# Kernel optimization log

Hardware: AMD Instinct MI355X
Metric: run time of the kernel (lower is better)

The kernel has to match this reference:

```python
import jax, jax.numpy as jnp
import numpy as np

EPS = 1e-05
NEG = -1000000000.0

def rmsnorm(x):
    var = jnp.mean(x * x, axis=-1, keepdims=True)
    return x * jax.lax.rsqrt(var + EPS)

def apply_rotary(x, cos, sin):
    # x: [B,T,H,D], cos/sin: [T,D]
    d = x.shape[-1]
    x1, x2 = x[..., : d // 2], x[..., d // 2 :]
    half_rot = jnp.concatenate([-x2, x1], axis=-1)
    c = cos[None, :, None, :]
    s = sin[None, :, None, :]
    return x * c + half_rot * s

def setup_inputs() -> dict:
    key = jax.random.key(0)
    ks = jax.random.split(key, 12)
    B, T, C, H = 2, 2048, 1024, 16
    hd = C // H
    std = 0.02
    return {
        "x": jax.random.normal(ks[0], (B, T, C), jnp.float32),
        "x0": jax.random.normal(ks[1], (B, T, C), jnp.float32),
        "lambdaResid": jnp.ones((), jnp.float32),
        "lambdaX0": jnp.ones((), jnp.float32),
        "cos": jax.random.uniform(ks[2], (T, hd), jnp.float32),
        "sin": jax.random.uniform(ks[3], (T, hd), jnp.float32),
        "qWeight": jax.random.normal(ks[4], (C, C), jnp.float32) * std,
        "kWeight": jax.random.normal(ks[5], (C, C), jnp.float32) * std,
        "vWeight": jax.random.normal(ks[6], (C, C), jnp.float32) * std,
        "projWeight": jax.random.normal(ks[7], (C, C), jnp.float32) * std,
        "fcWeight": jax.random.normal(ks[8], (C, 4 * C), jnp.float32) * std,
        "mlpProjWeight": jax.random.normal(ks[9], (4 * C, C), jnp.float32) * std,
    }

def reference(x, x0, lambdaResid, lambdaX0, cos, sin,
              qWeight, kWeight, vWeight, projWeight, fcWeight, mlpProjWeight):
    B, T, C = x.shape
    hd = cos.shape[-1]
    H = C // hd
    scaled = x * lambdaResid + x0 * lambdaX0
    pre = rmsnorm(scaled)
    q = (pre @ qWeight).reshape(B, T, H, hd)
    k = (pre @ kWeight).reshape(B, T, H, hd)
    v = (pre @ vWeight).reshape(B, T, H, hd)
    q = rmsnorm(apply_rotary(q, cos, sin))  # [B,T,H,D]
    k = rmsnorm(apply_rotary(k, cos, sin))
    scores = jnp.einsum('bthd,bshd->bhts', q, k) / jnp.sqrt(jnp.float32(hd))
    mask = jnp.tril(jnp.ones((T, T), bool))
    scores = jnp.where(mask[None, None], scores, NEG)
    probs = jax.nn.softmax(scores, axis=-1)
    attn = jnp.einsum('bhts,bshd->bthd', probs, v).reshape(B, T, C)
    scaled = scaled + attn @ projWeight
    h = rmsnorm(scaled) @ fcWeight
    h = jnp.square(jax.nn.relu(h))
    return scaled + h @ mlpProjWeight
```

## Files before the change

kernel.cpp:

```cpp
#include <hip/hip_runtime.h>
#include <hip/hip_bf16.h>
#include <stdint.h>

typedef _Float16 f16;
typedef __attribute__((ext_vector_type(8))) _Float16 f16x8;
typedef __attribute__((ext_vector_type(4))) _Float16 f16x4;
typedef __attribute__((ext_vector_type(2))) __fp16 fp16x2;
typedef __attribute__((ext_vector_type(4))) float f32x4;

__device__ __forceinline__ void g2l16(const void* g, void* l) {
  __builtin_amdgcn_global_load_lds(
      (const __attribute__((address_space(1))) uint32_t*)g,
      (__attribute__((address_space(3))) uint32_t*)l, 16, 0, 0);
}

__device__ __forceinline__ uint32_t pkrtz(float a, float b) {
  union { fp16x2 h; uint32_t u; } z;
  z.h = __builtin_amdgcn_cvt_pkrtz(a, b);
  return z.u;
}

__global__ __launch_bounds__(256)
void wconv_all_kernel(const float* __restrict__ Wq, const float* __restrict__ Wk,
                      const float* __restrict__ Wv, const float* __restrict__ Wp,
                      const float* __restrict__ Wfc, const float* __restrict__ Wmp,
                      f16* __restrict__ Dq, f16* __restrict__ Dk, f16* __restrict__ Dv,
                      f16* __restrict__ Dp, f16* __restrict__ Dfc, f16* __restrict__ Dmp)
{
  __shared__ float tile[32][33];
  int id = blockIdx.x;
  const float* W; f16* Wt; int K, N, local;
  if      (id < 1024) { W = Wq;  Wt = Dq;  K = 1024; N = 1024; local = id; }
  else if (id < 2048) { W = Wk;  Wt = Dk;  K = 1024; N = 1024; local = id - 1024; }
  else if (id < 3072) { W = Wv;  Wt = Dv;  K = 1024; N = 1024; local = id - 2048; }
  else if (id < 4096) { W = Wp;  Wt = Dp;  K = 1024; N = 1024; local = id - 3072; }
  else if (id < 8192) { W = Wfc; Wt = Dfc; K = 1024; N = 4096; local = id - 4096; }
  else                { W = Wmp; Wt = Dmp; K = 4096; N = 1024; local = id - 8192; }
  int ntx = N >> 5;
  int n0 = (local % ntx) * 32, k0 = (local / ntx) * 32;
  int tx = threadIdx.x & 31, ty = threadIdx.x >> 5;
#pragma unroll
  for (int i = 0; i < 4; ++i)
    tile[ty + 8*i][tx] = W[(size_t)(k0 + ty + 8*i) * N + (n0 + tx)];
  __syncthreads();
#pragma unroll
  for (int i = 0; i < 4; ++i)
    Wt[(size_t)(n0 + ty + 8*i) * K + (k0 + tx)] = (f16)tile[tx][ty + 8*i];
}

__global__ __launch_bounds__(256)
void scale_rms_kernel(const float* __restrict__ x, const float* __restrict__ x0,
                      const float* __restrict__ lamR, const float* __restrict__ lamX,
                      float* __restrict__ scaled, f16* __restrict__ pre)
{
  const int C = 1024;
  int row = blockIdx.x, tid = threadIdx.x;
  float lr = lamR[0], lx = lamX[0];
  size_t base = (size_t)row * C;
  float4 xv = ((const float4*)(x + base))[tid];
  float4 zv = ((const float4*)(x0 + base))[tid];
  float4 sv;
  sv.x = xv.x*lr + zv.x*lx;  sv.y = xv.y*lr + zv.y*lx;
  sv.z = xv.z*lr + zv.z*lx;  sv.w = xv.w*lr + zv.w*lx;
  float ss = sv.x*sv.x + sv.y*sv.y + sv.z*sv.z + sv.w*sv.w;
#pragma unroll
  for (int off = 32; off >= 1; off >>= 1) ss += __shfl_xor(ss, off);
  __shared__ float red[4];
  if ((tid & 63) == 0) red[tid >> 6] = ss;
  __syncthreads();
  float tot = red[0] + red[1] + red[2] + red[3];
  float rs = rsqrtf(tot * (1.0f / 1024.0f) + 1e-5f);
  ((float4*)(scaled + base))[tid] = sv;
  f16* p = pre + base + tid * 4;
  p[0] = (f16)(sv.x * rs); p[1] = (f16)(sv.y * rs);
  p[2] = (f16)(sv.z * rs); p[3] = (f16)(sv.w * rs);
}

__global__ __launch_bounds__(256)
void combine_rms_kernel(const float* __restrict__ resid, const f16* __restrict__ p0,
                        const f16* __restrict__ p1, float* __restrict__ scaled2,
                        f16* __restrict__ pre2)
{
  const int C = 1024;
  int row = blockIdx.x, tid = threadIdx.x;
  size_t base = (size_t)row * C;
  float4 rv = ((const float4*)(resid + base))[tid];
  f16x4 av = ((const f16x4*)(p0 + base))[tid];
  f16x4 bv = ((const f16x4*)(p1 + base))[tid];
  float4 sv;
  sv.x = rv.x + (float)av[0] + (float)bv[0];
  sv.y = rv.y + (float)av[1] + (float)bv[1];
  sv.z = rv.z + (float)av[2] + (float)bv[2];
  sv.w = rv.w + (float)av[3] + (float)bv[3];
  float ss = sv.x*sv.x + sv.y*sv.y + sv.z*sv.z + sv.w*sv.w;
#pragma unroll
  for (int off = 32; off >= 1; off >>= 1) ss += __shfl_xor(ss, off);
  __shared__ float red[4];
  if ((tid & 63) == 0) red[tid >> 6] = ss;
  __syncthreads();
  float tot = red[0] + red[1] + red[2] + red[3];
  float rs = rsqrtf(tot * (1.0f / 1024.0f) + 1e-5f);
  ((float4*)(scaled2 + base))[tid] = sv;
  f16* p = pre2 + base + tid * 4;
  p[0] = (f16)(sv.x * rs); p[1] = (f16)(sv.y * rs);
  p[2] = (f16)(sv.z * rs); p[3] = (f16)(sv.w * rs);
}

__global__ __launch_bounds__(256)
void combine_out4_kernel(const float* __restrict__ resid, const f16* __restrict__ parts,
                         size_t pstride, float* __restrict__ out)
{
  size_t i = (size_t)blockIdx.x * 256 + threadIdx.x;
  float4 rv = ((const float4*)resid)[i];
  float4 sv = rv;
#pragma unroll
  for (int z = 0; z < 4; ++z) {
    f16x4 av = ((const f16x4*)(parts + z * pstride))[i];
    sv.x += (float)av[0]; sv.y += (float)av[1];
    sv.z += (float)av[2]; sv.w += (float)av[3];
  }
  ((float4*)out)[i] = sv;
}

template<int EPI>
__global__ __launch_bounds__(256)
void gemm_kernel(const f16* __restrict__ A, const f16* __restrict__ Bt,
                 void* __restrict__ out, int M, int N, int K, int nb, int zb)
{
  __shared__ __align__(16) f16 smem[4 * 128 * 32];
  const int tid = threadIdx.x;
  const int wave = tid >> 6, lane = tid & 63;
  const int col = lane & 15, quad = lane >> 4;
  const int id = blockIdx.x;
  const int xcd = id & 7, s = id >> 3;
  const int n_i = s % nb;
  const int p = s / nb;
  const int mpx = (M >> 7) >> 3;
  const int zz = p / mpx;
  const int m_i = xcd * mpx + (p % mpx);
  const int m0 = m_i * 128, n0 = n_i * 128;
  const int wm = (wave >> 1) * 64, wn = (wave & 1) * 64;
  const int Ksub = K / zb;
  const int kBeg = zz * Ksub;
  const int nIter = Ksub >> 5;
  f32x4 acc[4][4] = {};

  const size_t rowb = (size_t)K * 2;
  const char* Agp = (const char*)A  + (size_t)m0 * rowb;
  const char* Bgp = (const char*)Bt + (size_t)n0 * rowb;

  const int r_st = (tid >> 2);
  const int cb_st = (tid & 3) << 4;
  const int lb0 = (wave * 64) << 4;
  const int lb1 = (256 + wave * 64) << 4;

#define STAGE(buf, k0)                                                           \
  {                                                                              \
    const size_t koff = (size_t)(k0) * 2;                                        \
    g2l16(Agp + (size_t)r_st * rowb + koff + cb_st,                              \
          (char*)smem + (buf) * 8192 + lb0);                                     \
    g2l16(Agp + (size_t)(r_st + 64) * rowb + koff + cb_st,                       \
          (char*)smem + (buf) * 8192 + lb1);                                     \
    g2l16(Bgp + (size_t)r_st * rowb + koff + cb_st,                              \
          (char*)smem + 16384 + (buf) * 8192 + lb0);                             \
    g2l16(Bgp + (size_t)(r_st + 64) * rowb + koff + cb_st,                       \
          (char*)smem + 16384 + (buf) * 8192 + lb1);                             \
  }

  STAGE(0, kBeg)
  for (int kt = 0; kt < nIter; ++kt) {
    __syncthreads();
    if (kt + 1 < nIter) STAGE((kt + 1) & 1, kBeg + (kt + 1) * 32)
    const f16* As = smem + (kt & 1) * 4096;
    const f16* Bs = smem + 8192 + (kt & 1) * 4096;
    f16x8 af[4], bf[4];
#pragma unroll
    for (int t = 0; t < 4; ++t)
      af[t] = *(const f16x8*)(As + (wm + t*16 + col) * 32 + quad * 8);
#pragma unroll
    for (int t = 0; t < 4; ++t)
      bf[t] = *(const f16x8*)(Bs + (wn + t*16 + col) * 32 + quad * 8);
#pragma unroll
    for (int mt = 0; mt < 4; ++mt)
#pragma unroll
      for (int nt = 0; nt < 4; ++nt)
        acc[mt][nt] = __builtin_amdgcn_mfma_f32_16x16x32_f16(af[mt], bf[nt], acc[mt][nt], 0, 0, 0);
  }
#undef STAGE
  f16* ep = smem + wave * 1024;
  f16* outz = (EPI == 4) ? ((f16*)out + (size_t)zz * M * N) : (f16*)out;
#pragma unroll
  for (int mt = 0; mt < 4; ++mt) {
#pragma unroll
    for (int nt = 0; nt < 4; ++nt) {
#pragma unroll
      for (int r = 0; r < 4; ++r) {
        float v = acc[mt][nt][r];
        if (EPI == 1) { float tv = v > 0.0f ? v : 0.0f; v = tv * tv; }
        ep[(quad * 4 + r) * 64 + ((nt ^ quad) * 16 + col)] = (f16)v;
      }
    }
#pragma unroll
    for (int j = 0; j < 2; ++j) {
      int e = j * 64 + lane;
      int row = e >> 3, rb = e & 7;
      int phys16 = (((rb >> 1) ^ (row >> 2)) << 1) + (rb & 1);
      f16x8 vv = *(const f16x8*)(ep + row * 64 + phys16 * 8);
      int grow = m0 + wm + mt * 16 + row;
      int gcol = n0 + wn + rb * 8;
      *(f16x8*)(outz + (size_t)grow * N + gcol) = vv;
    }
  }
}

__device__ __forceinline__ void stage256(const char* Agp, const char* Bgp, size_t rowb,
                                         char* lds, int st_r, size_t koff, int tid)
{
#pragma unroll
  for (int j = 0; j < 4; ++j) {
    g2l16(Agp + (size_t)(st_r + j * 64) * rowb + koff, lds + j * 8192 + tid * 16);
    g2l16(Bgp + (size_t)(st_r + j * 64) * rowb + koff, lds + 32768 + j * 8192 + tid * 16);
  }
}

template<int EPI>
__global__ __launch_bounds__(512, 2)
void gemm256_kernel(const f16* __restrict__ A, const f16* __restrict__ Bt,
                    void* __restrict__ out, int M, int N, int K, int nb, int zb)
{
  __shared__ __align__(16) f16 smem[65536];
  const int tid = threadIdx.x;
  const int wave = tid >> 6, lane = tid & 63;
  const int col = lane & 15, quad = lane >> 4;
  const int id = blockIdx.x;
  const int xcd = id & 7, sb = id >> 3;
  const int n_i = sb % nb;
  const int p = sb / nb;
  const int mpx = (M >> 8) >> 3;
  const int zz = p / mpx;
  const int m_i = xcd * mpx + (p % mpx);
  const int m0 = m_i * 256, n0 = n_i * 256;
  const int wm = (wave >> 2) * 128, wn = (wave & 3) * 64;
  const int Ksub = K / zb;
  const int kBeg = zz * Ksub;
  const int ntiles = Ksub >> 6;
  f32x4 acc[8][4] = {};

  const size_t rowb = (size_t)K * 2;
  const char* Agp = (const char*)A  + (size_t)m0 * rowb;
  const char* Bgp = (const char*)Bt + (size_t)n0 * rowb;

  const int st_r = tid >> 3;
  const size_t st_so = (size_t)(((tid & 7) ^ ((tid >> 3) & 7)) << 4);

  stage256(Agp, Bgp, rowb, (char*)smem,         st_r, (size_t)kBeg * 2 + st_so, tid);
  stage256(Agp, Bgp, rowb, (char*)smem + 65536, st_r, (size_t)(kBeg + 64) * 2 + st_so, tid);

  for (int t = 0; t < ntiles; ++t) {
    if (t < ntiles - 1) asm volatile("s_waitcnt vmcnt(8)" ::: "memory");
    else                asm volatile("s_waitcnt vmcnt(0)" ::: "memory");
    __builtin_amdgcn_s_barrier();
    asm volatile("" ::: "memory");

    const f16* As = smem + (t & 1) * 32768;
    const f16* Bs = As + 16384;
    f16x8 bf[4][2];
#pragma unroll
    for (int ct = 0; ct < 4; ++ct)
#pragma unroll
      for (int ks = 0; ks < 2; ++ks)
        bf[ct][ks] = *(const f16x8*)(Bs + (wn + ct*16 + col) * 64 +
                                     (((ks*4 + quad) ^ (col & 7)) << 3));
#pragma unroll
    for (int sp = 0; sp < 4; ++sp) {
      f16x8 af[2][2];
#pragma unroll
      for (int i = 0; i < 2; ++i)
#pragma unroll
        for (int ks = 0; ks < 2; ++ks)
          af[i][ks] = *(const f16x8*)(As + (wm + (sp*2 + i)*16 + col) * 64 +
                                      (((ks*4 + quad) ^ (col & 7)) << 3));
      __builtin_amdgcn_s_setprio(1);
#pragma unroll
      for (int i = 0; i < 2; ++i)
#pragma unroll
        for (int ct = 0; ct < 4; ++ct)
#pragma unroll
          for (int ks = 0; ks < 2; ++ks)
            acc[sp*2 + i][ct] = __builtin_amdgcn_mfma_f32_16x16x32_f16(
                af[i][ks], bf[ct][ks], acc[sp*2 + i][ct], 0, 0, 0);
      __builtin_amdgcn_s_setprio(0);
    }

    asm volatile("s_waitcnt lgkmcnt(0)" ::: "memory");
    __builtin_amdgcn_s_barrier();
    asm volatile("" ::: "memory");
    if (t + 2 < ntiles)
      stage256(Agp, Bgp, rowb, (char*)smem + (t & 1) * 65536, st_r,
               (size_t)(kBeg + (t + 2) * 64) * 2 + st_so, tid);
  }

  f16* ep = smem + wave * 1024;
  f16* outz = (EPI == 4) ? ((f16*)out + (size_t)zz * M * N) : (f16*)out;
#pragma unroll
  for (int mt = 0; mt < 8; ++mt) {
#pragma unroll
    for (int ct = 0; ct < 4; ++ct) {
#pragma unroll
      for (int r = 0; r < 4; ++r) {
        float v = acc[mt][ct][r];
        if (EPI == 1) { float tv = v > 0.0f ? v : 0.0f; v = tv * tv; }
        ep[(quad * 4 + r) * 64 + ((ct ^ quad) * 16 + col)] = (f16)v;
      }
    }
#pragma unroll
    for (int j = 0; j < 2; ++j) {
      int e = j * 64 + lane;
      int row = e >> 3, rb = e & 7;
      int phys16 = (((rb >> 1) ^ (row >> 2)) << 1) + (rb & 1);
      f16x8 vv = *(const f16x8*)(ep + row * 64 + phys16 * 8);
      int grow = m0 + wm + mt * 16 + row;
      int gcol = n0 + wn + rb * 8;
      *(f16x8*)(outz + (size_t)grow * N + gcol) = vv;
    }
  }
}

__global__ __launch_bounds__(512, 2)
void gemm256_qkv_kernel(const f16* __restrict__ A, const f16* __restrict__ Bt,
                        f16* __restrict__ qb, f16* __restrict__ kbuf, f16* __restrict__ vtg,
                        const float* __restrict__ cs, const float* __restrict__ sn)
{
  const int K = 1024, nb = 12, ntiles = 16;
  __shared__ __align__(16) f16 smem[65536];
  const int tid = threadIdx.x;
  const int wave = tid >> 6, lane = tid & 63;
  const int col = lane & 15, quad = lane >> 4;
  const int id = blockIdx.x;
  const int xcd = id & 7, sb = id >> 3;
  const int n_i = sb % nb;
  const int m_i = xcd * 2 + (sb / nb);
  const int m0 = m_i * 256, n0 = n_i * 256;
  const int wm = (wave >> 2) * 128, wn = (wave & 3) * 64;
  f32x4 acc[8][4] = {};

  const size_t rowb = (size_t)K * 2;
  const char* Agp = (const char*)A  + (size_t)m0 * rowb;
  const char* Bgp = (const char*)Bt + (size_t)n0 * rowb;

  const int st_r = tid >> 3;
  const size_t st_so = (size_t)(((tid & 7) ^ ((tid >> 3) & 7)) << 4);

  stage256(Agp, Bgp, rowb, (char*)smem,         st_r, st_so, tid);
  stage256(Agp, Bgp, rowb, (char*)smem + 65536, st_r, (size_t)64 * 2 + st_so, tid);

  for (int t = 0; t < ntiles; ++t) {
    if (t < ntiles - 1) asm volatile("s_waitcnt vmcnt(8)" ::: "memory");
    else                asm volatile("s_waitcnt vmcnt(0)" ::: "memory");
    __builtin_amdgcn_s_barrier();
    asm volatile("" ::: "memory");

    const f16* As = smem + (t & 1) * 32768;
    const f16* Bs = As + 16384;
    f16x8 bf[4][2];
#pragma unroll
    for (int ct = 0; ct < 4; ++ct)
#pragma unroll
      for (int ks = 0; ks < 2; ++ks)
        bf[ct][ks] = *(const f16x8*)(Bs + (wn + ct*16 + col) * 64 +
                                     (((ks*4 + quad) ^ (col & 7)) << 3));
#pragma unroll
    for (int sp = 0; sp < 4; ++sp) {
      f16x8 af[2][2];
#pragma unroll
      for (int i = 0; i < 2; ++i)
#pragma unroll
        for (int ks = 0; ks < 2; ++ks)
          af[i][ks] = *(const f16x8*)(As + (wm + (sp*2 + i)*16 + col) * 64 +
                                      (((ks*4 + quad) ^ (col & 7)) << 3));
      __builtin_amdgcn_s_setprio(1);
#pragma unroll
      for (int i = 0; i < 2; ++i)
#pragma unroll
        for (int ct = 0; ct < 4; ++ct)
#pragma unroll
          for (int ks = 0; ks < 2; ++ks)
            acc[sp*2 + i][ct] = __builtin_amdgcn_mfma_f32_16x16x32_f16(
                af[i][ks], bf[ct][ks], acc[sp*2 + i][ct], 0, 0, 0);
      __builtin_amdgcn_s_setprio(0);
    }

    asm volatile("s_waitcnt lgkmcnt(0)" ::: "memory");
    __builtin_amdgcn_s_barrier();
    asm volatile("" ::: "memory");
    if (t + 2 < ntiles)
      stage256(Agp, Bgp, rowb, (char*)smem + (t & 1) * 65536, st_r,
               (size_t)((t + 2) * 64) * 2 + st_so, tid);
  }

  const int cw = n0 + wn;
  const int sel = cw >> 10;
  if (sel < 2) {
    f16* dst = (sel == 0) ? qb : kbuf;
    const int cbase = cw & 1023;
    f16* ep = smem + wave * 1024;
#pragma unroll
    for (int mt = 0; mt < 8; ++mt) {
#pragma unroll
      for (int r = 0; r < 4; ++r) {
        const int t = (m0 + wm + mt * 16 + quad * 4 + r) & 2047;
        const float* cp = cs + t * 64 + col;
        const float* sp = sn + t * 64 + col;
        float yv[4];
        float ss = 0.f;
#pragma unroll
        for (int ct = 0; ct < 4; ++ct) {
          float c = cp[ct * 16], s = sp[ct * 16];
          float rot = acc[mt][ct ^ 2][r];
          float y = acc[mt][ct][r] * c + (ct < 2 ? -rot : rot) * s;
          yv[ct] = y;
          ss += y * y;
        }
        ss += __shfl_xor(ss, 1, 16);
        ss += __shfl_xor(ss, 2, 16);
        ss += __shfl_xor(ss, 4, 16);
        ss += __shfl_xor(ss, 8, 16);
        float rs = rsqrtf(ss * (1.0f / 64.0f) + 1e-5f);
#pragma unroll
        for (int ct = 0; ct < 4; ++ct) acc[mt][ct][r] = yv[ct] * rs;
      }
#pragma unroll
      for (int ct = 0; ct < 4; ++ct)
#pragma unroll
        for (int r = 0; r < 4; ++r)
          ep[(quad * 4 + r) * 64 + ((ct ^ quad) * 16 + col)] = (f16)acc[mt][ct][r];
#pragma unroll
      for (int j = 0; j < 2; ++j) {
        int e = j * 64 + lane;
        int row = e >> 3, rb = e & 7;
        int phys16 = (((rb >> 1) ^ (row >> 2)) << 1) + (rb & 1);
        f16x8 vv = *(const f16x8*)(ep + row * 64 + phys16 * 8);
        int grow = m0 + wm + mt * 16 + row;
        *(f16x8*)(dst + (size_t)grow * 1024 + cbase + rb * 8) = vv;
      }
    }
  } else {
#pragma unroll
    for (int mt = 0; mt < 8; ++mt) {
      int t0 = m0 + wm + mt * 16 + quad * 4;
      int b = t0 >> 11, t = t0 & 2047;
#pragma unroll
      for (int ct = 0; ct < 4; ++ct) {
        int dd = (cw & 1023) + ct * 16 + col;
        int hh = dd >> 6, d = dd & 63;
        f16x4 vv;
#pragma unroll
        for (int r = 0; r < 4; ++r) vv[r] = (f16)acc[mt][ct][r];
        *(f16x4*)(vtg + ((size_t)((b * 16 + hh) * 64 + d)) * 2048 + t) = vv;
      }
    }
  }
}

__global__ __launch_bounds__(512)
void attn_kernel(const f16* __restrict__ Q, const f16* __restrict__ Kc,
                 const f16* __restrict__ Vt, f16* __restrict__ O)
{
  const int T = 2048, C = 1024;
  __shared__ __align__(16) f16 Ks[2][64 * 64];
  __shared__ __align__(16) f16 Vs[2][64 * 64];
  const int tid = threadIdx.x, wave = tid >> 6, lane = tid & 63;
  const int col = lane & 15, quad = lane >> 4;
  const int bh = blockIdx.x, b = bh >> 4, h = bh & 15;
  const int pr = blockIdx.y;
  const int grp = wave >> 2;
  const int w4 = wave & 3;
  const int hiB = 31 - pr;
  const int myB = grp ? pr : hiB;
  const int q0 = myB * 64;

  const f16* qb = Q  + ((size_t)b * T) * C + h * 64;
  const f16* kb = Kc + ((size_t)b * T) * C + h * 64;
  const f16* vb = Vt + ((size_t)bh * 64) * T;

  f16x8 bq[2];
#pragma unroll
  for (int ks = 0; ks < 2; ++ks)
    bq[ks] = *(const f16x8*)(qb + (size_t)(q0 + w4*16 + col) * C + ks*32 + quad*8);

  f32x4 o_acc[4];
#pragma unroll
  for (int dt = 0; dt < 4; ++dt) o_acc[dt] = (f32x4){0.f,0.f,0.f,0.f};
  float l_acc = 0.f;

  const int srow = lane >> 3;
  const int sblk = (lane & 7) ^ srow;
  const int r0 = wave * 8;

  g2l16(kb + (size_t)(r0 + srow) * C + sblk * 8, (char*)Ks[0] + r0 * 128);
  g2l16(vb + (size_t)(r0 + srow) * T + sblk * 8, (char*)Vs[0] + r0 * 128);

  const int cm = col & 7;
  const int c00 = quad,            c01 = 4 + (quad ^ 1);
  const int c10 = 8 + (quad ^ 2),  c11 = 12 + (quad ^ 3);
  const int o00 = (((c00 >> 1) ^ cm) << 3) + ((c00 & 1) << 2);
  const int o01 = (((c01 >> 1) ^ cm) << 3) + ((c01 & 1) << 2);
  const int o10 = (((c10 >> 1) ^ cm) << 3) + ((c10 & 1) << 2);
  const int o11 = (((c11 >> 1) ^ cm) << 3) + ((c11 & 1) << 2);

  int cur = 0;
  for (int kt = 0; kt <= hiB; ++kt) {
    __syncthreads();

    if (kt < hiB) {
      const int ks1 = (kt + 1) * 64;
      g2l16(kb + (size_t)(ks1 + r0 + srow) * C + sblk * 8, (char*)Ks[cur ^ 1] + r0 * 128);
      g2l16(vb + (size_t)(r0 + srow) * T + ks1 + sblk * 8, (char*)Vs[cur ^ 1] + r0 * 128);
    }

    if (kt <= myB) {
      f32x4 s[4];
#pragma unroll
      for (int nt = 0; nt < 4; ++nt) s[nt] = (f32x4){0.f,0.f,0.f,0.f};
      __builtin_amdgcn_s_setprio(1);
#pragma unroll
      for (int ks = 0; ks < 2; ++ks) {
#pragma unroll
        for (int nt = 0; nt < 4; ++nt) {
          int key = nt * 16 + col;
          f16x8 ak = *(const f16x8*)(Ks[cur] + key * 64 + (((ks*4 + quad) ^ (key & 7)) * 8));
          s[nt] = __builtin_amdgcn_mfma_f32_16x16x32_f16(ak, bq[ks], s[nt], 0, 0, 0);
        }
      }
      __builtin_amdgcn_s_setprio(0);

      const bool masked = (kt == myB);
      const int qloc = w4 * 16 + col;
      uint32_t pk[4][2];
      float l_tile = 0.f;
#pragma unroll
      for (int nt = 0; nt < 4; ++nt) {
        float p[4];
#pragma unroll
        for (int r = 0; r < 4; ++r) {
          float pv = __expf(s[nt][r] * 0.125f);
          if (masked && (nt * 16 + quad * 4 + r > qloc)) pv = 0.0f;
          p[r] = pv;
        }
        l_tile += (p[0] + p[1]) + (p[2] + p[3]);
        pk[nt][0] = pkrtz(p[0], p[1]);
        pk[nt][1] = pkrtz(p[2], p[3]);
      }
      l_acc += l_tile;

      union { uint32_t u[4]; f16x8 v; } pa0, pa1;
      pa0.u[0] = pk[0][0];
      pa0.u[1] = pk[0][1];
      pa0.u[2] = (uint32_t)__shfl_xor((int)pk[1][0], 16);
      pa0.u[3] = (uint32_t)__shfl_xor((int)pk[1][1], 16);
      pa1.u[0] = (uint32_t)__shfl_xor((int)pk[2][0], 32);
      pa1.u[1] = (uint32_t)__shfl_xor((int)pk[2][1], 32);
      pa1.u[2] = (uint32_t)__shfl_xor((int)pk[3][0], 48);
      pa1.u[3] = (uint32_t)__shfl_xor((int)pk[3][1], 48);

      __builtin_amdgcn_s_setprio(1);
#pragma unroll
      for (int dt = 0; dt < 4; ++dt) {
        const f16* vrow = Vs[cur] + (dt * 16 + col) * 64;
        union { struct { f16x4 lo, hi; } p; f16x8 v; } bv0, bv1;
        bv0.p.lo = *(const f16x4*)(vrow + o00);
        bv0.p.hi = *(const f16x4*)(vrow + o01);
        bv1.p.lo = *(const f16x4*)(vrow + o10);
        bv1.p.hi = *(const f16x4*)(vrow + o11);
        o_acc[dt] = __builtin_amdgcn_mfma_f32_16x16x32_f16(pa0.v, bv0.v, o_acc[dt], 0, 0, 0);
        o_acc[dt] = __builtin_amdgcn_mfma_f32_16x16x32_f16(pa1.v, bv1.v, o_acc[dt], 0, 0, 0);
      }
      __builtin_amdgcn_s_setprio(0);
    }
    cur ^= 1;
  }

  l_acc += __shfl_xor(l_acc, 16);
  l_acc += __shfl_xor(l_acc, 32);
  float linv[4];
#pragma unroll
  for (int r = 0; r < 4; ++r)
    linv[r] = 1.0f / __shfl(l_acc, (wave & 4) * 16 + quad * 4 + r, 64);

#pragma unroll
  for (int dt = 0; dt < 4; ++dt) {
#pragma unroll
    for (int r = 0; r < 4; ++r) {
      int qr = q0 + w4 * 16 + quad * 4 + r;
      float v = o_acc[dt][r] * linv[r];
      O[((size_t)b * T + qr) * C + h * 64 + dt * 16 + col] = (f16)v;
    }
  }
}

extern "C" void kernel_launch(void* const* d_in, const int* in_sizes, int n_in,
                              void* d_out, int out_size, void* d_ws, size_t ws_size,
                              hipStream_t stream)
{
  const float* x    = (const float*)d_in[0];
  const float* x0   = (const float*)d_in[1];
  const float* lamR = (const float*)d_in[2];
  const float* lamX = (const float*)d_in[3];
  const float* cs   = (const float*)d_in[4];
  const float* sn   = (const float*)d_in[5];
  const float* Wq   = (const float*)d_in[6];
  const float* Wk   = (const float*)d_in[7];
  const float* Wv   = (const float*)d_in[8];
  const float* Wp   = (const float*)d_in[9];
  const float* Wfc  = (const float*)d_in[10];
  const float* Wmp  = (const float*)d_in[11];
  float* out = (float*)d_out;

  const int B = 2, T = 2048, C = 1024, H = 16;
  const int M = B * T;
  const size_t MB = 1ull << 20;
  char* ws = (char*)d_ws;
  f16*   Wqkv_t = (f16*)(ws + 0 * MB);
  f16*   Wp_t   = (f16*)(ws + 6 * MB);
  f16*   Wfc_t  = (f16*)(ws + 8 * MB);
  f16*   Wmp_t  = (f16*)(ws + 16 * MB);
  float* scaled  = (float*)(ws + 24 * MB);
  f16*   pre     = (f16*)(ws + 40 * MB);
  f16*   qb      = (f16*)(ws + 48 * MB);
  f16*   kbuf    = (f16*)(ws + 56 * MB);
  f16*   vtg     = (f16*)(ws + 64 * MB);
  float* scaled2 = (float*)(ws + 72 * MB);
  f16*   hbuf    = (f16*)(ws + 88 * MB);
  f16*   attnOut = pre;
  f16*   pre2    = qb;
  f16*   projP   = (f16*)(ws + 88 * MB);
  f16*   mlpP    = (f16*)(ws + 24 * MB);

  dim3 tb(256);
  dim3 tb5(512);
  wconv_all_kernel<<<dim3(12288), tb, 0, stream>>>(
      Wq, Wk, Wv, Wp, Wfc, Wmp,
      Wqkv_t, Wqkv_t + 1024*1024, Wqkv_t + 2048*1024, Wp_t, Wfc_t, Wmp_t);

  scale_rms_kernel<<<M, tb, 0, stream>>>(x, x0, lamR, lamX, scaled, pre);

  gemm256_qkv_kernel<<<dim3(192), tb5, 0, stream>>>(pre, Wqkv_t, qb, kbuf, vtg, cs, sn);

  attn_kernel<<<dim3(B * H, 16), tb5, 0, stream>>>(qb, kbuf, vtg, attnOut);

  gemm_kernel<4><<<dim3(8 * 32 * 2), tb, 0, stream>>>(attnOut, Wp_t, projP, M, C, C, 8, 2);
  combine_rms_kernel<<<M, tb, 0, stream>>>(scaled, projP, projP + (size_t)M*C, scaled2, pre2);

  gemm256_kernel<1><<<dim3(256), tb5, 0, stream>>>(pre2, Wfc_t, hbuf, M, 4*C, C, 16, 1);

  gemm256_kernel<4><<<dim3(256), tb5, 0, stream>>>(hbuf, Wmp_t, mlpP, M, C, 4*C, 4, 4);
  combine_out4_kernel<<<(M*C)/1024, tb, 0, stream>>>(scaled2, mlpP, (size_t)M*C, out);
}
```

Before: 335.4 us.

## Switch GEMM mainloops to 32-wide K tiles with a four-stage LDS ring

Both 256x256 GEMM kernels (the generic one and the fused QKV one) now stage K slices of 32 instead of 64, in a four-slot LDS ring that keeps three stages in flight. The next load is issued right after the top barrier rather than after the compute. The aim is deeper global-to-LDS latency hiding with the same LDS footprint. In exchange there are twice as many barriers per K, half as many MFMAs between them, and the XOR swizzle is dropped, so the 64-byte-stride LDS reads may hit bank conflicts.

```diff
diff --git a/kernel.cpp b/kernel.cpp
--- a/kernel.cpp
+++ b/kernel.cpp
@@ -213,14 +213,13 @@
   }
 }
 
-__device__ __forceinline__ void stage256(const char* Agp, const char* Bgp, size_t rowb,
-                                         char* lds, int st_r, size_t koff, int tid)
-{
-#pragma unroll
-  for (int j = 0; j < 4; ++j) {
-    g2l16(Agp + (size_t)(st_r + j * 64) * rowb + koff, lds + j * 8192 + tid * 16);
-    g2l16(Bgp + (size_t)(st_r + j * 64) * rowb + koff, lds + 32768 + j * 8192 + tid * 16);
-  }
+__device__ __forceinline__ void stage32(const char* Agp, const char* Bgp, size_t rowb,
+                                        char* lds, int r0s, int sl16, size_t koff, int tid)
+{
+  g2l16(Agp + (size_t)r0s * rowb + koff + sl16,         lds + tid * 16);
+  g2l16(Agp + (size_t)(r0s + 128) * rowb + koff + sl16, lds + 8192 + tid * 16);
+  g2l16(Bgp + (size_t)r0s * rowb + koff + sl16,         lds + 16384 + tid * 16);
+  g2l16(Bgp + (size_t)(r0s + 128) * rowb + koff + sl16, lds + 24576 + tid * 16);
 }
 
 template<int EPI>
@@ -243,61 +242,51 @@
   const int wm = (wave >> 2) * 128, wn = (wave & 3) * 64;
   const int Ksub = K / zb;
   const int kBeg = zz * Ksub;
-  const int ntiles = Ksub >> 6;
+  const int nt = Ksub >> 5;
   f32x4 acc[8][4] = {};
 
   const size_t rowb = (size_t)K * 2;
   const char* Agp = (const char*)A  + (size_t)m0 * rowb;
   const char* Bgp = (const char*)Bt + (size_t)n0 * rowb;
 
-  const int st_r = tid >> 3;
-  const size_t st_so = (size_t)(((tid & 7) ^ ((tid >> 3) & 7)) << 4);
-
-  stage256(Agp, Bgp, rowb, (char*)smem,         st_r, (size_t)kBeg * 2 + st_so, tid);
-  stage256(Agp, Bgp, rowb, (char*)smem + 65536, st_r, (size_t)(kBeg + 64) * 2 + st_so, tid);
-
-  for (int t = 0; t < ntiles; ++t) {
-    if (t < ntiles - 1) asm volatile("s_waitcnt vmcnt(8)" ::: "memory");
-    else                asm volatile("s_waitcnt vmcnt(0)" ::: "memory");
+  const int r0s = tid >> 2;
+  const int sl16 = (tid & 3) << 4;
+
+  stage32(Agp, Bgp, rowb, (char*)smem,         r0s, sl16, (size_t)kBeg * 2, tid);
+  stage32(Agp, Bgp, rowb, (char*)smem + 32768, r0s, sl16, (size_t)(kBeg + 32) * 2, tid);
+  stage32(Agp, Bgp, rowb, (char*)smem + 65536, r0s, sl16, (size_t)(kBeg + 64) * 2, tid);
+
+  for (int t = 0; t < nt; ++t) {
+    const int rem = nt - 1 - t;
+    if (rem >= 2)      asm volatile("s_waitcnt vmcnt(8)" ::: "memory");
+    else if (rem == 1) asm volatile("s_waitcnt vmcnt(4)" ::: "memory");
+    else               asm volatile("s_waitcnt vmcnt(0)" ::: "memory");
     __builtin_amdgcn_s_barrier();
     asm volatile("" ::: "memory");
 
-    const f16* As = smem + (t & 1) * 32768;
-    const f16* Bs = As + 16384;
-    f16x8 bf[4][2];
+    if (t + 3 < nt)
+      stage32(Agp, Bgp, rowb, (char*)smem + ((t + 3) & 3) * 32768, r0s, sl16,
+              (size_t)(kBeg + (t + 3) * 32) * 2, tid);
+
+    const f16* As = (const f16*)((const char*)smem + (t & 3) * 32768);
+    const f16* Bs = As + 8192;
+    f16x8 bf[4];
 #pragma unroll
     for (int ct = 0; ct < 4; ++ct)
-#pragma unroll
-      for (int ks = 0; ks < 2; ++ks)
-        bf[ct][ks] = *(const f16x8*)(Bs + (wn + ct*16 + col) * 64 +
-                                     (((ks*4 + quad) ^ (col & 7)) << 3));
-#pragma unroll
-    for (int sp = 0; sp < 4; ++sp) {
-      f16x8 af[2][2];
-#pragma unroll
-      for (int i = 0; i < 2; ++i)
-#pragma unroll
-        for (int ks = 0; ks < 2; ++ks)
-          af[i][ks] = *(const f16x8*)(As + (wm + (sp*2 + i)*16 + col) * 64 +
-                                      (((ks*4 + quad) ^ (col & 7)) << 3));
-      __builtin_amdgcn_s_setprio(1);
-#pragma unroll
-      for (int i = 0; i < 2; ++i)
-#pragma unroll
-        for (int ct = 0; ct < 4; ++ct)
-#pragma unroll
-          for (int ks = 0; ks < 2; ++ks)
-            acc[sp*2 + i][ct] = __builtin_amdgcn_mfma_f32_16x16x32_f16(
-                af[i][ks], bf[ct][ks], acc[sp*2 + i][ct], 0, 0, 0);
-      __builtin_amdgcn_s_setprio(0);
-    }
+      bf[ct] = *(const f16x8*)(Bs + (wn + ct*16 + col) * 32 + quad * 8);
+    __builtin_amdgcn_s_setprio(1);
+#pragma unroll
+    for (int mt = 0; mt < 8; ++mt) {
+      f16x8 af = *(const f16x8*)(As + (wm + mt*16 + col) * 32 + quad * 8);
+#pragma unroll
+      for (int ct = 0; ct < 4; ++ct)
+        acc[mt][ct] = __builtin_amdgcn_mfma_f32_16x16x32_f16(af, bf[ct], acc[mt][ct], 0, 0, 0);
+    }
+    __builtin_amdgcn_s_setprio(0);
 
     asm volatile("s_waitcnt lgkmcnt(0)" ::: "memory");
     __builtin_amdgcn_s_barrier();
     asm volatile("" ::: "memory");
-    if (t + 2 < ntiles)
-      stage256(Agp, Bgp, rowb, (char*)smem + (t & 1) * 65536, st_r,
-               (size_t)(kBeg + (t + 2) * 64) * 2 + st_so, tid);
   }
 
   f16* ep = smem + wave * 1024;
@@ -331,7 +320,7 @@
                         f16* __restrict__ qb, f16* __restrict__ kbuf, f16* __restrict__ vtg,
                         const float* __restrict__ cs, const float* __restrict__ sn)
 {
-  const int K = 1024, nb = 12, ntiles = 16;
+  const int K = 1024, nb = 12, nt = 32;
   __shared__ __align__(16) f16 smem[65536];
   const int tid = threadIdx.x;
   const int wave = tid >> 6, lane = tid & 63;
@@ -348,54 +337,44 @@
   const char* Agp = (const char*)A  + (size_t)m0 * rowb;
   const char* Bgp = (const char*)Bt + (size_t)n0 * rowb;
 
-  const int st_r = tid >> 3;
-  const size_t st_so = (size_t)(((tid & 7) ^ ((tid >> 3) & 7)) << 4);
-
-  stage256(Agp, Bgp, rowb, (char*)smem,         st_r, st_so, tid);
-  stage256(Agp, Bgp, rowb, (char*)smem + 65536, st_r, (size_t)64 * 2 + st_so, tid);
-
-  for (int t = 0; t < ntiles; ++t) {
-    if (t < ntiles - 1) asm volatile("s_waitcnt vmcnt(8)" ::: "memory");
-    else                asm volatile("s_waitcnt vmcnt(0)" ::: "memory");
+  const int r0s = tid >> 2;
+  const int sl16 = (tid & 3) << 4;
+
+  stage32(Agp, Bgp, rowb, (char*)smem,         r0s, sl16, 0, tid);
+  stage32(Agp, Bgp, rowb, (char*)smem + 32768, r0s, sl16, (size_t)32 * 2, tid);
+  stage32(Agp, Bgp, rowb, (char*)smem + 65536, r0s, sl16, (size_t)64 * 2, tid);
+
+  for (int t = 0; t < nt; ++t) {
+    const int rem = nt - 1 - t;
+    if (rem >= 2)      asm volatile("s_waitcnt vmcnt(8)" ::: "memory");
+    else if (rem == 1) asm volatile("s_waitcnt vmcnt(4)" ::: "memory");
+    else               asm volatile("s_waitcnt vmcnt(0)" ::: "memory");
     __builtin_amdgcn_s_barrier();
     asm volatile("" ::: "memory");
 
-    const f16* As = smem + (t & 1) * 32768;
-    const f16* Bs = As + 16384;
-    f16x8 bf[4][2];
+    if (t + 3 < nt)
+      stage32(Agp, Bgp, rowb, (char*)smem + ((t + 3) & 3) * 32768, r0s, sl16,
+              (size_t)((t + 3) * 32) * 2, tid);
+
+    const f16* As = (const f16*)((const char*)smem + (t & 3) * 32768);
+    const f16* Bs = As + 8192;
+    f16x8 bf[4];
 #pragma unroll
     for (int ct = 0; ct < 4; ++ct)
-#pragma unroll
-      for (int ks = 0; ks < 2; ++ks)
-        bf[ct][ks] = *(const f16x8*)(Bs + (wn + ct*16 + col) * 64 +
-                                     (((ks*4 + quad) ^ (col & 7)) << 3));
-#pragma unroll
-    for (int sp = 0; sp < 4; ++sp) {
-      f16x8 af[2][2];
-#pragma unroll
-      for (int i = 0; i < 2; ++i)
-#pragma unroll
-        for (int ks = 0; ks < 2; ++ks)
-          af[i][ks] = *(const f16x8*)(As + (wm + (sp*2 + i)*16 + col) * 64 +
-                                      (((ks*4 + quad) ^ (col & 7)) << 3));
-      __builtin_amdgcn_s_setprio(1);
-#pragma unroll
-      for (int i = 0; i < 2; ++i)
-#pragma unroll
-        for (int ct = 0; ct < 4; ++ct)
-#pragma unroll
-          for (int ks = 0; ks < 2; ++ks)
-            acc[sp*2 + i][ct] = __builtin_amdgcn_mfma_f32_16x16x32_f16(
-                af[i][ks], bf[ct][ks], acc[sp*2 + i][ct], 0, 0, 0);
-      __builtin_amdgcn_s_setprio(0);
-    }
+      bf[ct] = *(const f16x8*)(Bs + (wn + ct*16 + col) * 32 + quad * 8);
+    __builtin_amdgcn_s_setprio(1);
+#pragma unroll
+    for (int mt = 0; mt < 8; ++mt) {
+      f16x8 af = *(const f16x8*)(As + (wm + mt*16 + col) * 32 + quad * 8);
+#pragma unroll
+      for (int ct = 0; ct < 4; ++ct)
+        acc[mt][ct] = __builtin_amdgcn_mfma_f32_16x16x32_f16(af, bf[ct], acc[mt][ct], 0, 0, 0);
+    }
+    __builtin_amdgcn_s_setprio(0);
 
     asm volatile("s_waitcnt lgkmcnt(0)" ::: "memory");
     __builtin_amdgcn_s_barrier();
     asm volatile("" ::: "memory");
-    if (t + 2 < ntiles)
-      stage256(Agp, Bgp, rowb, (char*)smem + (t & 1) * 65536, st_r,
-               (size_t)((t + 2) * 64) * 2 + st_so, tid);
   }
 
   const int cw = n0 + wn;
```

After: 337.5 us. No clear change (+0.6%).
